# Kernel tuning notes

Measured on AMD Instinct MI355X. Metric: run time of the kernel, lower is better.

The kernel has to match this reference:

```python
import jax, jax.numpy as jnp
from jax import lax
import numpy as np

STATE_DIM = 64
CHANNELS = 128
SEQ_LEN = 4096
BATCH = 16
DT_MIN, DT_MAX = 1e-3, 1e-1


def hippo(n):
    # HiPPO-LegS construction, matching the torch staticmethod
    ar = jnp.arange(n, dtype=jnp.float32)
    P = jnp.sqrt(1.0 + 2.0 * ar)
    A = P[:, None] * P[None, :]
    A = jnp.tril(A) - jnp.diag(ar)
    B = jnp.sqrt(2.0 * ar + 1.0)
    return -A, B[:, None]


def setup_inputs() -> dict:
    key = jax.random.key(0)
    k_u, k_c = jax.random.split(key)
    A, B = hippo(STATE_DIM)
    # xavier_normal_ for C: std = sqrt(2/(fan_in+fan_out))
    std = float(np.sqrt(2.0 / (CHANNELS + STATE_DIM)))
    C = jax.random.normal(k_c, (CHANNELS, STATE_DIM), dtype=jnp.float32) * std
    D = jnp.ones((CHANNELS, 1), dtype=jnp.float32)
    # deterministic dt at log-midpoint of [dt_min, dt_max]
    dt = jnp.exp(jnp.array([(np.log(DT_MIN) + np.log(DT_MAX)) / 2.0], dtype=jnp.float32))
    u = jax.random.normal(k_u, (BATCH, SEQ_LEN), dtype=jnp.float32)
    return {"u": u, "A": A, "B": B, "C": C, "D": D, "dt": dt}


def reference(u, A, B, C, D, dt):
    # Training-path forward of LinearStateSpaceLayer (conv-kernel construction + conv1d)
    b, L = u.shape
    n = A.shape[0]
    dt_s = dt[0]
    I = jnp.eye(n, dtype=A.dtype)
    BL = jnp.linalg.inv(I - 0.5 * dt_s * A)            # bilinear discretization
    A_bar = BL @ (I + 0.5 * dt_s * A)                  # (n, n)
    B_bar = (BL * dt_s) @ B                            # (n, 1)

    # kernel k[j] = C @ A_bar^j @ B_bar for j = 0..L-1, via a scan of matvecs
    def step(v, _):
        return A_bar @ v, v
    _, vs = lax.scan(step, B_bar[:, 0], None, length=L)  # (L, n), vs[j] = A_bar^j B_bar
    k_causal = vs @ C.T                                  # (L, channels)
    # torch ordering: k_conv[c, 0, i] = C A_bar^{L-1-i} B_bar = k_causal[L-1-i, c]
    k_conv = k_causal[::-1].T[:, None, :]                # (channels, 1, L)

    # torch F.conv1d is cross-correlation; lax conv_general_dilated matches
    y = lax.conv_general_dilated(
        u[:, None, :], k_conv,
        window_strides=(1,), padding=[(L - 1, L - 1)],
        dimension_numbers=("NCH", "OIH", "NCH"),
    )[:, :, :L]                                          # (b, channels, L)

    # skip term: (u.unsqueeze(-1) @ D.T).transpose(-1,-2) == u[b,t] * D[c,0]
    y = y + u[:, None, :] * D[None, :, :]                # (b, channels, L)
    return y
```

## Files before the change

### kernel.cpp

```cpp
#include <hip/hip_runtime.h>

#define NS   64
#define CH   128
#define LSEQ 4096
#define NB   16
#define SCH  64
#define MCH  64
#define ST   68
#define CT_ST 132

#define WS_ABAR 0
#define WS_A16  4096
#define WS_VS   8192
#define WS_BBAR 12288

#define X0_IDX(b, m) (((size_t)(b) * CH) * LSEQ + (size_t)(m) * SCH)

#define FMA44(av, bv)                                                          \
    a0.x += av.x * bv.x; a0.y += av.x * bv.y; a0.z += av.x * bv.z; a0.w += av.x * bv.w; \
    a1.x += av.y * bv.x; a1.y += av.y * bv.y; a1.z += av.y * bv.z; a1.w += av.y * bv.w; \
    a2.x += av.z * bv.x; a2.y += av.z * bv.y; a2.z += av.z * bv.z; a2.w += av.z * bv.w; \
    a3.x += av.w * bv.x; a3.y += av.w * bv.y; a3.z += av.w * bv.z; a3.w += av.w * bv.w;

__global__ __launch_bounds__(256) void k_sb(const float* __restrict__ u,
                                            const float* __restrict__ A,
                                            const float* __restrict__ Bv,
                                            const float* __restrict__ dtp,
                                            float* __restrict__ ws,
                                            float* __restrict__ out) {
    __shared__ __align__(16) float Mrow[NS * ST];
    __shared__ __align__(16) float Mcol[(NS + 1) * ST];
    __shared__ __align__(16) float Nrow[NS * ST];
    __shared__ __align__(16) float Ncol[NS * ST];
    __shared__ __align__(16) float VT[NS * ST];
    __shared__ __align__(16) float vsS[NS * NS];
    __shared__ __align__(16) float xleS[MCH * NS];
    __shared__ __align__(16) float part[2][4 * NS];
    __shared__ __align__(16) float bcol[NS];
    __shared__ float rdiag[NS], xcS[NS], vtmp[NS];
    const int tid = threadIdx.x;
    const int b = blockIdx.x;
    const float dt = dtp[0];
    const float hdt = 0.5f * dt;

    for (int o = tid; o < NS * ST; o += 256) { Mrow[o] = 0.f; Nrow[o] = 0.f; Ncol[o] = 0.f; VT[o] = 0.f; }
    for (int o = tid; o < (NS + 1) * ST; o += 256) Mcol[o] = 0.f;
    __syncthreads();

    for (int o = tid; o < NS * NS; o += 256) {
        int i = o >> 6, k = o & 63;
        float a = A[o];
        float d = (i == k) ? 1.0f : 0.0f;
        Nrow[i * ST + k] = d - hdt * a;
        Ncol[k * ST + i] = d + hdt * a;
    }
    if (tid < NS) bcol[tid] = dt * Bv[tid];
    __syncthreads();
    if (tid < NS) rdiag[tid] = 1.0f / Nrow[tid * ST + tid];
    __syncthreads();

    if (tid <= NS) {
        const int j = tid;
        float* xrow = &Mcol[j * ST];
        for (int I = 0; I < 16; ++I) {
            const int i0 = 4 * I;
            float4 t2 = (j < NS) ? *(const float4*)&Ncol[j * ST + i0]
                                 : *(const float4*)&bcol[i0];
            float a0 = t2.x, a1 = t2.y, a2 = t2.z, a3 = t2.w;
            for (int k = 0; k < i0; k += 4) {
                float4 xk = *(const float4*)&xrow[k];
                float4 n0 = *(const float4*)&Nrow[(i0 + 0) * ST + k];
                float4 n1 = *(const float4*)&Nrow[(i0 + 1) * ST + k];
                float4 n2 = *(const float4*)&Nrow[(i0 + 2) * ST + k];
                float4 n3 = *(const float4*)&Nrow[(i0 + 3) * ST + k];
                a0 -= n0.x * xk.x + n0.y * xk.y + n0.z * xk.z + n0.w * xk.w;
                a1 -= n1.x * xk.x + n1.y * xk.y + n1.z * xk.z + n1.w * xk.w;
                a2 -= n2.x * xk.x + n2.y * xk.y + n2.z * xk.z + n2.w * xk.w;
                a3 -= n3.x * xk.x + n3.y * xk.y + n3.z * xk.z + n3.w * xk.w;
            }
            float4 rd  = *(const float4*)&rdiag[i0];
            float4 nb1 = *(const float4*)&Nrow[(i0 + 1) * ST + i0];
            float4 nb2 = *(const float4*)&Nrow[(i0 + 2) * ST + i0];
            float4 nb3 = *(const float4*)&Nrow[(i0 + 3) * ST + i0];
            float x0 = a0 * rd.x;
            float x1 = (a1 - nb1.x * x0) * rd.y;
            float x2 = (a2 - nb2.x * x0 - nb2.y * x1) * rd.z;
            float x3 = (a3 - nb3.x * x0 - nb3.y * x1 - nb3.z * x2) * rd.w;
            float4 xw = {x0, x1, x2, x3};
            *(float4*)&xrow[i0] = xw;
        }
    }
    __syncthreads();

    {
        const int i0 = 4 * (tid >> 4), j0 = 4 * (tid & 15);
        float4 r0 = *(const float4*)&Mcol[(j0 + 0) * ST + i0];
        float4 r1 = *(const float4*)&Mcol[(j0 + 1) * ST + i0];
        float4 r2 = *(const float4*)&Mcol[(j0 + 2) * ST + i0];
        float4 r3 = *(const float4*)&Mcol[(j0 + 3) * ST + i0];
        float4 w0 = {r0.x, r1.x, r2.x, r3.x};
        float4 w1 = {r0.y, r1.y, r2.y, r3.y};
        float4 w2 = {r0.z, r1.z, r2.z, r3.z};
        float4 w3 = {r0.w, r1.w, r2.w, r3.w};
        *(float4*)&Mrow[(i0 + 0) * ST + j0] = w0;
        *(float4*)&Mrow[(i0 + 1) * ST + j0] = w1;
        *(float4*)&Mrow[(i0 + 2) * ST + j0] = w2;
        *(float4*)&Mrow[(i0 + 3) * ST + j0] = w3;
        if (b == 0) {
            *(float4*)&ws[WS_ABAR + (i0 + 0) * NS + j0] = w0;
            *(float4*)&ws[WS_ABAR + (i0 + 1) * NS + j0] = w1;
            *(float4*)&ws[WS_ABAR + (i0 + 2) * NS + j0] = w2;
            *(float4*)&ws[WS_ABAR + (i0 + 3) * NS + j0] = w3;
        }
    }
    if (b == 0 && tid < 16)
        *(float4*)&ws[WS_BBAR + 4 * tid] = *(const float4*)&Mcol[NS * ST + 4 * tid];
    __syncthreads();

    if ((tid >> 6) == 0) {
        const int i = tid;
        float v = Mcol[NS * ST + i];
        vtmp[i] = v;
        VT[i * ST + 0] = v;
        for (int j = 1; j < 4; ++j) {
            __threadfence_block();
            float s = 0.f;
            for (int k = 0; k < NS; k += 4) {
                float4 ar = *(const float4*)&Mrow[i * ST + k];
                float4 vv = *(const float4*)&vtmp[k];
                s += ar.x * vv.x + ar.y * vv.y + ar.z * vv.z + ar.w * vv.w;
            }
            __threadfence_block();
            vtmp[i] = s;
            VT[i * ST + j] = s;
        }
    }
    __syncthreads();

    float *cm = Mrow, *cmt = Mcol, *nm = Nrow, *nmt = Ncol;
    const int w4 = tid >> 6, l = tid & 63;
    const int si0 = 16 * w4 + 4 * (l >> 4);
    const int sj0 = 4 * (l & 15);
    const int skmax = 16 * (w4 + 1);
    for (int s = 1; s <= 6; ++s) {
        {
            float4 a0 = {0,0,0,0}, a1 = {0,0,0,0}, a2 = {0,0,0,0}, a3 = {0,0,0,0};
            for (int k = 0; k < skmax; k += 4) {
                float4 av0 = *(const float4*)&cmt[(k + 0) * ST + si0];
                float4 bv0 = *(const float4*)&cm [(k + 0) * ST + sj0];
                float4 av1 = *(const float4*)&cmt[(k + 1) * ST + si0];
                float4 bv1 = *(const float4*)&cm [(k + 1) * ST + sj0];
                float4 av2 = *(const float4*)&cmt[(k + 2) * ST + si0];
                float4 bv2 = *(const float4*)&cm [(k + 2) * ST + sj0];
                float4 av3 = *(const float4*)&cmt[(k + 3) * ST + si0];
                float4 bv3 = *(const float4*)&cm [(k + 3) * ST + sj0];
                FMA44(av0, bv0)
                FMA44(av1, bv1)
                FMA44(av2, bv2)
                FMA44(av3, bv3)
            }
            *(float4*)&nm[(si0 + 0) * ST + sj0] = a0;
            *(float4*)&nm[(si0 + 1) * ST + sj0] = a1;
            *(float4*)&nm[(si0 + 2) * ST + sj0] = a2;
            *(float4*)&nm[(si0 + 3) * ST + sj0] = a3;
            float4 t0 = {a0.x, a1.x, a2.x, a3.x};
            float4 t1 = {a0.y, a1.y, a2.y, a3.y};
            float4 t2 = {a0.z, a1.z, a2.z, a3.z};
            float4 t3 = {a0.w, a1.w, a2.w, a3.w};
            *(float4*)&nmt[(sj0 + 0) * ST + si0] = t0;
            *(float4*)&nmt[(sj0 + 1) * ST + si0] = t1;
            *(float4*)&nmt[(sj0 + 2) * ST + si0] = t2;
            *(float4*)&nmt[(sj0 + 3) * ST + si0] = t3;
        }
        __syncthreads();
        { float* t = cm; cm = nm; nm = t; t = cmt; cmt = nmt; nmt = t; }
        if (s == 4 && b == 0) {
            for (int o = tid; o < (NS * NS) / 4; o += 256) {
                int r = o >> 4, c4 = (o & 15) * 4;
                *(float4*)&ws[WS_A16 + r * NS + c4] = *(const float4*)&cm[r * ST + c4];
            }
        }
        if (s >= 2 && s <= 5) {
            const int m = 1 << s;
            if (tid < 4 * m) {
                const int vi = 4 * (tid & 15), vj = 4 * (tid >> 4);
                float4 a0 = {0,0,0,0}, a1 = {0,0,0,0}, a2 = {0,0,0,0}, a3 = {0,0,0,0};
                for (int k = 0; k < NS; k += 2) {
                    float4 av  = *(const float4*)&cmt[k * ST + vi];
                    float4 bv  = *(const float4*)&VT [k * ST + vj];
                    float4 av2 = *(const float4*)&cmt[(k + 1) * ST + vi];
                    float4 bv2 = *(const float4*)&VT [(k + 1) * ST + vj];
                    FMA44(av, bv)
                    FMA44(av2, bv2)
                }
                *(float4*)&VT[(vi + 0) * ST + vj + m] = a0;
                *(float4*)&VT[(vi + 1) * ST + vj + m] = a1;
                *(float4*)&VT[(vi + 2) * ST + vj + m] = a2;
                *(float4*)&VT[(vi + 3) * ST + vj + m] = a3;
            }
        }
        __syncthreads();
    }

    {
        const int it = tid >> 4, jt = tid & 15;
        const int i0 = 4 * it, j0 = 4 * jt;
        float4 v0 = *(const float4*)&VT[(i0 + 0) * ST + j0];
        float4 v1 = *(const float4*)&VT[(i0 + 1) * ST + j0];
        float4 v2 = *(const float4*)&VT[(i0 + 2) * ST + j0];
        float4 v3 = *(const float4*)&VT[(i0 + 3) * ST + j0];
        float4 w0 = {v0.x, v1.x, v2.x, v3.x};
        float4 w1 = {v0.y, v1.y, v2.y, v3.y};
        float4 w2 = {v0.z, v1.z, v2.z, v3.z};
        float4 w3 = {v0.w, v1.w, v2.w, v3.w};
        *(float4*)&vsS[(j0 + 0) * NS + i0] = w0;
        *(float4*)&vsS[(j0 + 1) * NS + i0] = w1;
        *(float4*)&vsS[(j0 + 2) * NS + i0] = w2;
        *(float4*)&vsS[(j0 + 3) * NS + i0] = w3;
        if (b == 0) {
            *(float4*)&ws[WS_VS + (j0 + 0) * NS + i0] = w0;
            *(float4*)&ws[WS_VS + (j0 + 1) * NS + i0] = w1;
            *(float4*)&ws[WS_VS + (j0 + 2) * NS + i0] = w2;
            *(float4*)&ws[WS_VS + (j0 + 3) * NS + i0] = w3;
        }
    }

    {
        const int jj = tid & 63;
        for (int rep = 0; rep < 4; ++rep) {
            const int m0 = 4 * (tid >> 6) + 16 * rep;
            float4 v;
            v.x = u[b * LSEQ + (m0 + 0) * SCH + 63 - jj];
            v.y = u[b * LSEQ + (m0 + 1) * SCH + 63 - jj];
            v.z = u[b * LSEQ + (m0 + 2) * SCH + 63 - jj];
            v.w = u[b * LSEQ + (m0 + 3) * SCH + 63 - jj];
            *(float4*)&Nrow[jj * ST + m0] = v;
        }
    }
    const int i = tid & 63, q = tid >> 6;
    float4 a64[4];
#pragma unroll
    for (int kq = 0; kq < 4; ++kq)
        a64[kq] = *(const float4*)&Mrow[i * ST + 16 * q + 4 * kq];
    __syncthreads();

    {
        const int ig = tid & 15, mg = tid >> 4;
        float4 a0 = {0,0,0,0}, a1 = {0,0,0,0}, a2 = {0,0,0,0}, a3 = {0,0,0,0};
        for (int j = 0; j < NS; j += 2) {
            float4 am  = *(const float4*)&Nrow[j * ST + 4 * mg];
            float4 bi  = *(const float4*)&vsS[j * NS + 4 * ig];
            float4 am2 = *(const float4*)&Nrow[(j + 1) * ST + 4 * mg];
            float4 bi2 = *(const float4*)&vsS[(j + 1) * NS + 4 * ig];
            FMA44(am, bi)
            FMA44(am2, bi2)
        }
        *(float4*)&xleS[(4 * mg + 0) * NS + 4 * ig] = a0;
        *(float4*)&xleS[(4 * mg + 1) * NS + 4 * ig] = a1;
        *(float4*)&xleS[(4 * mg + 2) * NS + 4 * ig] = a2;
        *(float4*)&xleS[(4 * mg + 3) * NS + 4 * ig] = a3;
    }
    if (tid < NS) xcS[tid] = 0.f;
    __syncthreads();

    for (int m = 0; m < MCH; ++m) {
        if (q == 0) out[X0_IDX(b, m) + i] = xcS[i];
        float4 t0 = *(const float4*)(xcS + 16 * q + 0);
        float4 t1 = *(const float4*)(xcS + 16 * q + 4);
        float4 t2 = *(const float4*)(xcS + 16 * q + 8);
        float4 t3 = *(const float4*)(xcS + 16 * q + 12);
        float s = a64[0].x * t0.x + a64[0].y * t0.y + a64[0].z * t0.z + a64[0].w * t0.w
                + a64[1].x * t1.x + a64[1].y * t1.y + a64[1].z * t1.z + a64[1].w * t1.w
                + a64[2].x * t2.x + a64[2].y * t2.y + a64[2].z * t2.z + a64[2].w * t2.w
                + a64[3].x * t3.x + a64[3].y * t3.y + a64[3].z * t3.z + a64[3].w * t3.w;
        part[m & 1][q * 64 + i] = s;
        __syncthreads();
        float xn = part[m & 1][i] + part[m & 1][64 + i] + part[m & 1][128 + i]
                 + part[m & 1][192 + i] + xleS[m * 64 + i];
        xcS[i] = xn;
    }
}

__global__ __launch_bounds__(256) void k_main2(const float* __restrict__ u,
                                               const float* __restrict__ Cm,
                                               const float* __restrict__ Dv,
                                               const float* __restrict__ ws,
                                               float* __restrict__ out) {
    __shared__ __align__(16) float Xl[NS * ST];
    __shared__ __align__(16) float CtS[NS * CT_ST];
    __shared__ __align__(16) float xcW[4 * NS];
    __shared__ __align__(16) float xbS[4 * NS];
    __shared__ __align__(16) float VSS[16 * NS];
    __shared__ __align__(16) float pleS[4 * NS];
    __shared__ __align__(16) float partS[4 * NS];
    __shared__ float uS[SCH], DS[CH], bbS[NS];
    const int m = blockIdx.x, b = blockIdx.y;
    const int tid = threadIdx.x;
    const int l = tid & 63, w = tid >> 6;

    for (int o = tid; o < (NS * NS) / 4; o += 256) {
        int r = o >> 4, c4 = (o & 15) * 4;
        *(float4*)&Xl[r * ST + c4]     = *(const float4*)&ws[WS_ABAR + r * NS + c4];
        *(float4*)&CtS[r * CT_ST + c4] = *(const float4*)&ws[WS_A16 + r * NS + c4];
    }
    for (int o = tid; o < 16 * NS; o += 256) VSS[o] = ws[WS_VS + o];
    if (tid < NS) {
        uS[tid]  = u[b * LSEQ + m * SCH + tid];
        bbS[tid] = ws[WS_BBAR + tid];
        xbS[tid] = out[X0_IDX(b, m) + tid];
    }
    if (tid < CH) DS[tid] = Dv[tid];
    __syncthreads();

    const int r0 = l & 15, q = l >> 4;
    float4 ar[4][4];
#pragma unroll
    for (int b4 = 0; b4 < 4; ++b4)
#pragma unroll
        for (int kq = 0; kq < 4; ++kq)
            ar[b4][kq] = *(const float4*)&Xl[(r0 + 16 * b4) * ST + 16 * q + 4 * kq];
    float bbr[4];
#pragma unroll
    for (int b4 = 0; b4 < 4; ++b4) bbr[b4] = bbS[r0 + 16 * b4];
    float4 a16r[4];
#pragma unroll
    for (int kq = 0; kq < 4; ++kq)
        a16r[kq] = *(const float4*)&CtS[l * CT_ST + 16 * w + 4 * kq];

    {
        float s = 0.f;
#pragma unroll
        for (int j = 0; j < 16; ++j) s += VSS[j * NS + l] * uS[16 * w + 15 - j];
        pleS[w * NS + l] = s;
    }
    __syncthreads();

    for (int p = 1; p < 4; ++p) {
        float4 x0q = *(const float4*)&xbS[(p - 1) * NS + 16 * w + 0];
        float4 x1q = *(const float4*)&xbS[(p - 1) * NS + 16 * w + 4];
        float4 x2q = *(const float4*)&xbS[(p - 1) * NS + 16 * w + 8];
        float4 x3q = *(const float4*)&xbS[(p - 1) * NS + 16 * w + 12];
        float s = a16r[0].x * x0q.x + a16r[0].y * x0q.y + a16r[0].z * x0q.z + a16r[0].w * x0q.w
                + a16r[1].x * x1q.x + a16r[1].y * x1q.y + a16r[1].z * x1q.z + a16r[1].w * x1q.w
                + a16r[2].x * x2q.x + a16r[2].y * x2q.y + a16r[2].z * x2q.z + a16r[2].w * x2q.w
                + a16r[3].x * x3q.x + a16r[3].y * x3q.y + a16r[3].z * x3q.z + a16r[3].w * x3q.w;
        partS[w * NS + l] = s;
        __syncthreads();
        if (w == 0) {
            float xn = partS[l] + partS[NS + l] + partS[2 * NS + l] + partS[3 * NS + l]
                     + pleS[(p - 1) * NS + l];
            xbS[p * NS + l] = xn;
        }
        __syncthreads();
    }

    xcW[w * NS + l] = xbS[w * NS + l];
    for (int s = 0; s < 16; ++s) {
        __threadfence_block();
        const int t = 16 * w + s;
        float4 x0q = *(const float4*)&xcW[w * NS + 16 * q + 0];
        float4 x1q = *(const float4*)&xcW[w * NS + 16 * q + 4];
        float4 x2q = *(const float4*)&xcW[w * NS + 16 * q + 8];
        float4 x3q = *(const float4*)&xcW[w * NS + 16 * q + 12];
        float p0, p1, p2, p3;
        p0 = ar[0][0].x * x0q.x + ar[0][0].y * x0q.y + ar[0][0].z * x0q.z + ar[0][0].w * x0q.w
           + ar[0][1].x * x1q.x + ar[0][1].y * x1q.y + ar[0][1].z * x1q.z + ar[0][1].w * x1q.w
           + ar[0][2].x * x2q.x + ar[0][2].y * x2q.y + ar[0][2].z * x2q.z + ar[0][2].w * x2q.w
           + ar[0][3].x * x3q.x + ar[0][3].y * x3q.y + ar[0][3].z * x3q.z + ar[0][3].w * x3q.w;
        p1 = ar[1][0].x * x0q.x + ar[1][0].y * x0q.y + ar[1][0].z * x0q.z + ar[1][0].w * x0q.w
           + ar[1][1].x * x1q.x + ar[1][1].y * x1q.y + ar[1][1].z * x1q.z + ar[1][1].w * x1q.w
           + ar[1][2].x * x2q.x + ar[1][2].y * x2q.y + ar[1][2].z * x2q.z + ar[1][2].w * x2q.w
           + ar[1][3].x * x3q.x + ar[1][3].y * x3q.y + ar[1][3].z * x3q.z + ar[1][3].w * x3q.w;
        p2 = ar[2][0].x * x0q.x + ar[2][0].y * x0q.y + ar[2][0].z * x0q.z + ar[2][0].w * x0q.w
           + ar[2][1].x * x1q.x + ar[2][1].y * x1q.y + ar[2][1].z * x1q.z + ar[2][1].w * x1q.w
           + ar[2][2].x * x2q.x + ar[2][2].y * x2q.y + ar[2][2].z * x2q.z + ar[2][2].w * x2q.w
           + ar[2][3].x * x3q.x + ar[2][3].y * x3q.y + ar[2][3].z * x3q.z + ar[2][3].w * x3q.w;
        p3 = ar[3][0].x * x0q.x + ar[3][0].y * x0q.y + ar[3][0].z * x0q.z + ar[3][0].w * x0q.w
           + ar[3][1].x * x1q.x + ar[3][1].y * x1q.y + ar[3][1].z * x1q.z + ar[3][1].w * x1q.w
           + ar[3][2].x * x2q.x + ar[3][2].y * x2q.y + ar[3][2].z * x2q.z + ar[3][2].w * x2q.w
           + ar[3][3].x * x3q.x + ar[3][3].y * x3q.y + ar[3][3].z * x3q.z + ar[3][3].w * x3q.w;
        p0 += __shfl_xor(p0, 16, 64); p1 += __shfl_xor(p1, 16, 64);
        p2 += __shfl_xor(p2, 16, 64); p3 += __shfl_xor(p3, 16, 64);
        p0 += __shfl_xor(p0, 32, 64); p1 += __shfl_xor(p1, 32, 64);
        p2 += __shfl_xor(p2, 32, 64); p3 += __shfl_xor(p3, 32, 64);
        const float ut = uS[t];
        p0 += bbr[0] * ut; p1 += bbr[1] * ut; p2 += bbr[2] * ut; p3 += bbr[3] * ut;
        const float xv = (q == 0) ? p0 : (q == 1) ? p1 : (q == 2) ? p2 : p3;
        const int row = r0 + 16 * q;
        xcW[w * NS + row] = xv;
        Xl[row * ST + t]  = xv;
    }
    __syncthreads();

    for (int rep = 0; rep < 8; ++rep) {
        const int ii = tid & 63;
        const int cg = (tid >> 6) + 4 * rep;
        float4 v;
        v.x = Cm[(4 * cg + 0) * NS + ii];
        v.y = Cm[(4 * cg + 1) * NS + ii];
        v.z = Cm[(4 * cg + 2) * NS + ii];
        v.w = Cm[(4 * cg + 3) * NS + ii];
        *(float4*)&CtS[ii * CT_ST + 4 * cg] = v;
    }
    __syncthreads();

    {
        const int tg = tid & 7, cq = tid >> 3;
        float acc[4][8];
#pragma unroll
        for (int r = 0; r < 4; ++r)
#pragma unroll
            for (int c = 0; c < 8; ++c) acc[r][c] = 0.f;
#pragma unroll 4
        for (int ii = 0; ii < NS; ++ii) {
            float4 cv = *(const float4*)&CtS[ii * CT_ST + 4 * cq];
            float4 xa = *(const float4*)&Xl[ii * ST + 8 * tg + 0];
            float4 xb = *(const float4*)&Xl[ii * ST + 8 * tg + 4];
            float cr[4] = {cv.x, cv.y, cv.z, cv.w};
            float xv[8] = {xa.x, xa.y, xa.z, xa.w, xb.x, xb.y, xb.z, xb.w};
#pragma unroll
            for (int r = 0; r < 4; ++r)
#pragma unroll
                for (int c = 0; c < 8; ++c) acc[r][c] += cr[r] * xv[c];
        }
        const size_t obase = ((size_t)b * CH) * LSEQ + (size_t)m * SCH + 8 * tg;
#pragma unroll
        for (int r = 0; r < 4; ++r) {
            const int c = 4 * cq + r;
            const float dv = DS[c];
            float4 o1, o2;
            o1.x = acc[r][0] + dv * uS[8 * tg + 0];
            o1.y = acc[r][1] + dv * uS[8 * tg + 1];
            o1.z = acc[r][2] + dv * uS[8 * tg + 2];
            o1.w = acc[r][3] + dv * uS[8 * tg + 3];
            o2.x = acc[r][4] + dv * uS[8 * tg + 4];
            o2.y = acc[r][5] + dv * uS[8 * tg + 5];
            o2.z = acc[r][6] + dv * uS[8 * tg + 6];
            o2.w = acc[r][7] + dv * uS[8 * tg + 7];
            float* op = out + obase + (size_t)c * LSEQ;
            *(float4*)(op)     = o1;
            *(float4*)(op + 4) = o2;
        }
    }
}

extern "C" void kernel_launch(void* const* d_in, const int* in_sizes, int n_in,
                              void* d_out, int out_size, void* d_ws, size_t ws_size,
                              hipStream_t stream) {
    const float* u   = (const float*)d_in[0];
    const float* A   = (const float*)d_in[1];
    const float* Bv  = (const float*)d_in[2];
    const float* Cm  = (const float*)d_in[3];
    const float* Dv  = (const float*)d_in[4];
    const float* dtp = (const float*)d_in[5];
    float* ws  = (float*)d_ws;
    float* out = (float*)d_out;

    k_sb<<<NB, 256, 0, stream>>>(u, A, Bv, dtp, ws, out);
    k_main2<<<dim3(MCH, NB), 256, 0, stream>>>(u, Cm, Dv, ws, out);
}
```

Measured before the change: 167.7 us.

## Overlap Krylov vector build with matrix squaring using extra warps in setup kernel

The setup kernel goes to 512 threads. The upper 256 threads compute the A_bar^j B_bar columns (VT) while the lower 256 square the matrix, which removes the serial 4-step matvec phase and one barrier per squaring step. The triangular solve now keeps its row in registers, and the diagonal reciprocal is computed straight from A. In the second kernel several shared buffers are aliased into one pool to cut LDS use, at the cost of losing the padded stride for the C-transpose tile, which may add bank conflicts.

```diff
diff --git a/kernel.cpp b/kernel.cpp
--- a/kernel.cpp
+++ b/kernel.cpp
@@ -7,7 +7,7 @@
 #define SCH  64
 #define MCH  64
 #define ST   68
-#define CT_ST 132
+#define CP   128
 
 #define WS_ABAR 0
 #define WS_A16  4096
@@ -15,6 +15,13 @@
 #define WS_BBAR 12288
 
 #define X0_IDX(b, m) (((size_t)(b) * CH) * LSEQ + (size_t)(m) * SCH)
+
+#define P_VSS  0
+#define P_XCW  1024
+#define P_XBS  1280
+#define P_PLE  1536
+#define P_PART 1792
+#define P_A16  2048
 
 #define FMA44(av, bv)                                                          \
     a0.x += av.x * bv.x; a0.y += av.x * bv.y; a0.z += av.x * bv.z; a0.w += av.x * bv.w; \
@@ -22,7 +29,7 @@
     a2.x += av.z * bv.x; a2.y += av.z * bv.y; a2.z += av.z * bv.z; a2.w += av.z * bv.w; \
     a3.x += av.w * bv.x; a3.y += av.w * bv.y; a3.z += av.w * bv.z; a3.w += av.w * bv.w;
 
-__global__ __launch_bounds__(256) void k_sb(const float* __restrict__ u,
+__global__ __launch_bounds__(512) void k_sb(const float* __restrict__ u,
                                             const float* __restrict__ A,
                                             const float* __restrict__ Bv,
                                             const float* __restrict__ dtp,
@@ -37,46 +44,47 @@
     __shared__ __align__(16) float xleS[MCH * NS];
     __shared__ __align__(16) float part[2][4 * NS];
     __shared__ __align__(16) float bcol[NS];
-    __shared__ float rdiag[NS], xcS[NS], vtmp[NS];
+    __shared__ float rdiag[NS], xcS[NS];
     const int tid = threadIdx.x;
     const int b = blockIdx.x;
     const float dt = dtp[0];
     const float hdt = 0.5f * dt;
 
-    for (int o = tid; o < NS * ST; o += 256) { Mrow[o] = 0.f; Nrow[o] = 0.f; Ncol[o] = 0.f; VT[o] = 0.f; }
-    for (int o = tid; o < (NS + 1) * ST; o += 256) Mcol[o] = 0.f;
-    __syncthreads();
-
-    for (int o = tid; o < NS * NS; o += 256) {
+    for (int o = tid; o < NS * ST; o += 512) { Mrow[o] = 0.f; Nrow[o] = 0.f; Ncol[o] = 0.f; VT[o] = 0.f; }
+    for (int o = tid; o < (NS + 1) * ST; o += 512) Mcol[o] = 0.f;
+    __syncthreads();
+
+    for (int o = tid; o < NS * NS; o += 512) {
         int i = o >> 6, k = o & 63;
         float a = A[o];
         float d = (i == k) ? 1.0f : 0.0f;
         Nrow[i * ST + k] = d - hdt * a;
         Ncol[k * ST + i] = d + hdt * a;
     }
-    if (tid < NS) bcol[tid] = dt * Bv[tid];
-    __syncthreads();
-    if (tid < NS) rdiag[tid] = 1.0f / Nrow[tid * ST + tid];
+    if (tid < NS) {
+        bcol[tid]  = dt * Bv[tid];
+        rdiag[tid] = 1.0f / (1.0f - hdt * A[tid * NS + tid]);
+    }
     __syncthreads();
 
     if (tid <= NS) {
-        const int j = tid;
-        float* xrow = &Mcol[j * ST];
+        float xr[NS];
+        const float* t2b = (tid < NS) ? &Ncol[tid * ST] : bcol;
+#pragma unroll
         for (int I = 0; I < 16; ++I) {
             const int i0 = 4 * I;
-            float4 t2 = (j < NS) ? *(const float4*)&Ncol[j * ST + i0]
-                                 : *(const float4*)&bcol[i0];
+            float4 t2 = *(const float4*)&t2b[i0];
             float a0 = t2.x, a1 = t2.y, a2 = t2.z, a3 = t2.w;
+#pragma unroll
             for (int k = 0; k < i0; k += 4) {
-                float4 xk = *(const float4*)&xrow[k];
                 float4 n0 = *(const float4*)&Nrow[(i0 + 0) * ST + k];
                 float4 n1 = *(const float4*)&Nrow[(i0 + 1) * ST + k];
                 float4 n2 = *(const float4*)&Nrow[(i0 + 2) * ST + k];
                 float4 n3 = *(const float4*)&Nrow[(i0 + 3) * ST + k];
-                a0 -= n0.x * xk.x + n0.y * xk.y + n0.z * xk.z + n0.w * xk.w;
-                a1 -= n1.x * xk.x + n1.y * xk.y + n1.z * xk.z + n1.w * xk.w;
-                a2 -= n2.x * xk.x + n2.y * xk.y + n2.z * xk.z + n2.w * xk.w;
-                a3 -= n3.x * xk.x + n3.y * xk.y + n3.z * xk.z + n3.w * xk.w;
+                a0 -= n0.x * xr[k] + n0.y * xr[k + 1] + n0.z * xr[k + 2] + n0.w * xr[k + 3];
+                a1 -= n1.x * xr[k] + n1.y * xr[k + 1] + n1.z * xr[k + 2] + n1.w * xr[k + 3];
+                a2 -= n2.x * xr[k] + n2.y * xr[k + 1] + n2.z * xr[k + 2] + n2.w * xr[k + 3];
+                a3 -= n3.x * xr[k] + n3.y * xr[k + 1] + n3.z * xr[k + 2] + n3.w * xr[k + 3];
             }
             float4 rd  = *(const float4*)&rdiag[i0];
             float4 nb1 = *(const float4*)&Nrow[(i0 + 1) * ST + i0];
@@ -86,13 +94,18 @@
             float x1 = (a1 - nb1.x * x0) * rd.y;
             float x2 = (a2 - nb2.x * x0 - nb2.y * x1) * rd.z;
             float x3 = (a3 - nb3.x * x0 - nb3.y * x1 - nb3.z * x2) * rd.w;
-            float4 xw = {x0, x1, x2, x3};
-            *(float4*)&xrow[i0] = xw;
-        }
-    }
-    __syncthreads();
-
-    {
+            xr[i0 + 0] = x0; xr[i0 + 1] = x1; xr[i0 + 2] = x2; xr[i0 + 3] = x3;
+        }
+        float* xrow = &Mcol[tid * ST];
+#pragma unroll
+        for (int k = 0; k < NS; k += 4) {
+            float4 v = {xr[k], xr[k + 1], xr[k + 2], xr[k + 3]};
+            *(float4*)&xrow[k] = v;
+        }
+    }
+    __syncthreads();
+
+    if (tid < 256) {
         const int i0 = 4 * (tid >> 4), j0 = 4 * (tid & 15);
         float4 r0 = *(const float4*)&Mcol[(j0 + 0) * ST + i0];
         float4 r1 = *(const float4*)&Mcol[(j0 + 1) * ST + i0];
@@ -115,37 +128,18 @@
     }
     if (b == 0 && tid < 16)
         *(float4*)&ws[WS_BBAR + 4 * tid] = *(const float4*)&Mcol[NS * ST + 4 * tid];
-    __syncthreads();
-
-    if ((tid >> 6) == 0) {
-        const int i = tid;
-        float v = Mcol[NS * ST + i];
-        vtmp[i] = v;
-        VT[i * ST + 0] = v;
-        for (int j = 1; j < 4; ++j) {
-            __threadfence_block();
-            float s = 0.f;
+    if (tid < NS) VT[tid * ST + 0] = Mcol[NS * ST + tid];
+    __syncthreads();
+
+    float *cm = Mrow, *cmt = Mcol, *nm = Nrow, *nmt = Ncol;
+    const int l = tid & 63;
+    const int si0 = 16 * ((tid >> 6) & 3) + 4 * (l >> 4);
+    const int sj0 = 4 * (l & 15);
+    for (int s = 1; s <= 6; ++s) {
+        if (tid < 256) {
+            float4 a0 = {0,0,0,0}, a1 = {0,0,0,0}, a2 = {0,0,0,0}, a3 = {0,0,0,0};
+#pragma unroll 4
             for (int k = 0; k < NS; k += 4) {
-                float4 ar = *(const float4*)&Mrow[i * ST + k];
-                float4 vv = *(const float4*)&vtmp[k];
-                s += ar.x * vv.x + ar.y * vv.y + ar.z * vv.z + ar.w * vv.w;
-            }
-            __threadfence_block();
-            vtmp[i] = s;
-            VT[i * ST + j] = s;
-        }
-    }
-    __syncthreads();
-
-    float *cm = Mrow, *cmt = Mcol, *nm = Nrow, *nmt = Ncol;
-    const int w4 = tid >> 6, l = tid & 63;
-    const int si0 = 16 * w4 + 4 * (l >> 4);
-    const int sj0 = 4 * (l & 15);
-    const int skmax = 16 * (w4 + 1);
-    for (int s = 1; s <= 6; ++s) {
-        {
-            float4 a0 = {0,0,0,0}, a1 = {0,0,0,0}, a2 = {0,0,0,0}, a3 = {0,0,0,0};
-            for (int k = 0; k < skmax; k += 4) {
                 float4 av0 = *(const float4*)&cmt[(k + 0) * ST + si0];
                 float4 bv0 = *(const float4*)&cm [(k + 0) * ST + sj0];
                 float4 av1 = *(const float4*)&cmt[(k + 1) * ST + si0];
@@ -171,40 +165,56 @@
             *(float4*)&nmt[(sj0 + 1) * ST + si0] = t1;
             *(float4*)&nmt[(sj0 + 2) * ST + si0] = t2;
             *(float4*)&nmt[(sj0 + 3) * ST + si0] = t3;
+        } else {
+            const int e = tid - 256;
+            if (s == 1) {
+                if (e < NS) {
+                    float sum = 0.f;
+#pragma unroll 8
+                    for (int k = 0; k < NS; ++k) sum += cmt[k * ST + e] * VT[k * ST + 0];
+                    VT[e * ST + 1] = sum;
+                }
+            } else if (s == 2) {
+                if (e < 2 * NS) {
+                    const int i = e & 63, j = e >> 6;
+                    float sum = 0.f;
+#pragma unroll 8
+                    for (int k = 0; k < NS; ++k) sum += cmt[k * ST + i] * VT[k * ST + j];
+                    VT[i * ST + 2 + j] = sum;
+                }
+            } else {
+                const int mexp = 1 << (s - 1);
+                if (e < 4 * mexp) {
+                    const int vi = 4 * (e & 15), vj = 4 * (e >> 4);
+                    float4 a0 = {0,0,0,0}, a1 = {0,0,0,0}, a2 = {0,0,0,0}, a3 = {0,0,0,0};
+#pragma unroll 4
+                    for (int k = 0; k < NS; k += 2) {
+                        float4 av  = *(const float4*)&cmt[k * ST + vi];
+                        float4 bv  = *(const float4*)&VT [k * ST + vj];
+                        float4 av2 = *(const float4*)&cmt[(k + 1) * ST + vi];
+                        float4 bv2 = *(const float4*)&VT [(k + 1) * ST + vj];
+                        FMA44(av, bv)
+                        FMA44(av2, bv2)
+                    }
+                    *(float4*)&VT[(vi + 0) * ST + vj + mexp] = a0;
+                    *(float4*)&VT[(vi + 1) * ST + vj + mexp] = a1;
+                    *(float4*)&VT[(vi + 2) * ST + vj + mexp] = a2;
+                    *(float4*)&VT[(vi + 3) * ST + vj + mexp] = a3;
+                }
+            }
         }
         __syncthreads();
         { float* t = cm; cm = nm; nm = t; t = cmt; cmt = nmt; nmt = t; }
         if (s == 4 && b == 0) {
-            for (int o = tid; o < (NS * NS) / 4; o += 256) {
+            for (int o = tid; o < (NS * NS) / 4; o += 512) {
                 int r = o >> 4, c4 = (o & 15) * 4;
                 *(float4*)&ws[WS_A16 + r * NS + c4] = *(const float4*)&cm[r * ST + c4];
             }
         }
-        if (s >= 2 && s <= 5) {
-            const int m = 1 << s;
-            if (tid < 4 * m) {
-                const int vi = 4 * (tid & 15), vj = 4 * (tid >> 4);
-                float4 a0 = {0,0,0,0}, a1 = {0,0,0,0}, a2 = {0,0,0,0}, a3 = {0,0,0,0};
-                for (int k = 0; k < NS; k += 2) {
-                    float4 av  = *(const float4*)&cmt[k * ST + vi];
-                    float4 bv  = *(const float4*)&VT [k * ST + vj];
-                    float4 av2 = *(const float4*)&cmt[(k + 1) * ST + vi];
-                    float4 bv2 = *(const float4*)&VT [(k + 1) * ST + vj];
-                    FMA44(av, bv)
-                    FMA44(av2, bv2)
-                }
-                *(float4*)&VT[(vi + 0) * ST + vj + m] = a0;
-                *(float4*)&VT[(vi + 1) * ST + vj + m] = a1;
-                *(float4*)&VT[(vi + 2) * ST + vj + m] = a2;
-                *(float4*)&VT[(vi + 3) * ST + vj + m] = a3;
-            }
-        }
-        __syncthreads();
-    }
-
-    {
-        const int it = tid >> 4, jt = tid & 15;
-        const int i0 = 4 * it, j0 = 4 * jt;
+    }
+
+    if (tid < 256) {
+        const int i0 = 4 * (tid >> 4), j0 = 4 * (tid & 15);
         float4 v0 = *(const float4*)&VT[(i0 + 0) * ST + j0];
         float4 v1 = *(const float4*)&VT[(i0 + 1) * ST + j0];
         float4 v2 = *(const float4*)&VT[(i0 + 2) * ST + j0];
@@ -224,11 +234,11 @@
             *(float4*)&ws[WS_VS + (j0 + 3) * NS + i0] = w3;
         }
     }
-
     {
         const int jj = tid & 63;
-        for (int rep = 0; rep < 4; ++rep) {
-            const int m0 = 4 * (tid >> 6) + 16 * rep;
+#pragma unroll
+        for (int rep = 0; rep < 2; ++rep) {
+            const int m0 = 4 * (tid >> 6) + 32 * rep;
             float4 v;
             v.x = u[b * LSEQ + (m0 + 0) * SCH + 63 - jj];
             v.y = u[b * LSEQ + (m0 + 1) * SCH + 63 - jj];
@@ -237,16 +247,20 @@
             *(float4*)&Nrow[jj * ST + m0] = v;
         }
     }
-    const int i = tid & 63, q = tid >> 6;
+    const int i = tid & 63, q = (tid >> 6) & 3;
     float4 a64[4];
-#pragma unroll
-    for (int kq = 0; kq < 4; ++kq)
-        a64[kq] = *(const float4*)&Mrow[i * ST + 16 * q + 4 * kq];
-    __syncthreads();
-
-    {
+    if (tid < 256) {
+#pragma unroll
+        for (int kq = 0; kq < 4; ++kq)
+            a64[kq] = *(const float4*)&Mrow[i * ST + 16 * q + 4 * kq];
+    }
+    if (tid < NS) xcS[tid] = 0.f;
+    __syncthreads();
+
+    if (tid < 256) {
         const int ig = tid & 15, mg = tid >> 4;
         float4 a0 = {0,0,0,0}, a1 = {0,0,0,0}, a2 = {0,0,0,0}, a3 = {0,0,0,0};
+#pragma unroll 4
         for (int j = 0; j < NS; j += 2) {
             float4 am  = *(const float4*)&Nrow[j * ST + 4 * mg];
             float4 bi  = *(const float4*)&vsS[j * NS + 4 * ig];
@@ -260,24 +274,27 @@
         *(float4*)&xleS[(4 * mg + 2) * NS + 4 * ig] = a2;
         *(float4*)&xleS[(4 * mg + 3) * NS + 4 * ig] = a3;
     }
-    if (tid < NS) xcS[tid] = 0.f;
     __syncthreads();
 
     for (int m = 0; m < MCH; ++m) {
-        if (q == 0) out[X0_IDX(b, m) + i] = xcS[i];
-        float4 t0 = *(const float4*)(xcS + 16 * q + 0);
-        float4 t1 = *(const float4*)(xcS + 16 * q + 4);
-        float4 t2 = *(const float4*)(xcS + 16 * q + 8);
-        float4 t3 = *(const float4*)(xcS + 16 * q + 12);
-        float s = a64[0].x * t0.x + a64[0].y * t0.y + a64[0].z * t0.z + a64[0].w * t0.w
-                + a64[1].x * t1.x + a64[1].y * t1.y + a64[1].z * t1.z + a64[1].w * t1.w
-                + a64[2].x * t2.x + a64[2].y * t2.y + a64[2].z * t2.z + a64[2].w * t2.w
-                + a64[3].x * t3.x + a64[3].y * t3.y + a64[3].z * t3.z + a64[3].w * t3.w;
-        part[m & 1][q * 64 + i] = s;
+        if (tid < 256) {
+            if (q == 0 && tid < 64) out[X0_IDX(b, m) + i] = xcS[i];
+            float4 t0 = *(const float4*)(xcS + 16 * q + 0);
+            float4 t1 = *(const float4*)(xcS + 16 * q + 4);
+            float4 t2 = *(const float4*)(xcS + 16 * q + 8);
+            float4 t3 = *(const float4*)(xcS + 16 * q + 12);
+            float s = a64[0].x * t0.x + a64[0].y * t0.y + a64[0].z * t0.z + a64[0].w * t0.w
+                    + a64[1].x * t1.x + a64[1].y * t1.y + a64[1].z * t1.z + a64[1].w * t1.w
+                    + a64[2].x * t2.x + a64[2].y * t2.y + a64[2].z * t2.z + a64[2].w * t2.w
+                    + a64[3].x * t3.x + a64[3].y * t3.y + a64[3].z * t3.z + a64[3].w * t3.w;
+            part[m & 1][q * 64 + i] = s;
+        }
         __syncthreads();
-        float xn = part[m & 1][i] + part[m & 1][64 + i] + part[m & 1][128 + i]
-                 + part[m & 1][192 + i] + xleS[m * 64 + i];
-        xcS[i] = xn;
+        if (tid < 256) {
+            float xn = part[m & 1][i] + part[m & 1][64 + i] + part[m & 1][128 + i]
+                     + part[m & 1][192 + i] + xleS[m * 64 + i];
+            xcS[i] = xn;
+        }
     }
 }
 
@@ -287,12 +304,7 @@
                                                const float* __restrict__ ws,
                                                float* __restrict__ out) {
     __shared__ __align__(16) float Xl[NS * ST];
-    __shared__ __align__(16) float CtS[NS * CT_ST];
-    __shared__ __align__(16) float xcW[4 * NS];
-    __shared__ __align__(16) float xbS[4 * NS];
-    __shared__ __align__(16) float VSS[16 * NS];
-    __shared__ __align__(16) float pleS[4 * NS];
-    __shared__ __align__(16) float partS[4 * NS];
+    __shared__ __align__(16) float pool[NS * CP];
     __shared__ float uS[SCH], DS[CH], bbS[NS];
     const int m = blockIdx.x, b = blockIdx.y;
     const int tid = threadIdx.x;
@@ -300,14 +312,14 @@
 
     for (int o = tid; o < (NS * NS) / 4; o += 256) {
         int r = o >> 4, c4 = (o & 15) * 4;
-        *(float4*)&Xl[r * ST + c4]     = *(const float4*)&ws[WS_ABAR + r * NS + c4];
-        *(float4*)&CtS[r * CT_ST + c4] = *(const float4*)&ws[WS_A16 + r * NS + c4];
-    }
-    for (int o = tid; o < 16 * NS; o += 256) VSS[o] = ws[WS_VS + o];
+        *(float4*)&Xl[r * ST + c4]          = *(const float4*)&ws[WS_ABAR + r * NS + c4];
+        *(float4*)&pool[P_A16 + r * NS + c4] = *(const float4*)&ws[WS_A16 + r * NS + c4];
+    }
+    for (int o = tid; o < 16 * NS; o += 256) pool[P_VSS + o] = ws[WS_VS + o];
     if (tid < NS) {
         uS[tid]  = u[b * LSEQ + m * SCH + tid];
         bbS[tid] = ws[WS_BBAR + tid];
-        xbS[tid] = out[X0_IDX(b, m) + tid];
+        pool[P_XBS + tid] = out[X0_IDX(b, m) + tid];
     }
     if (tid < CH) DS[tid] = Dv[tid];
     __syncthreads();
@@ -325,43 +337,43 @@
     float4 a16r[4];
 #pragma unroll
     for (int kq = 0; kq < 4; ++kq)
-        a16r[kq] = *(const float4*)&CtS[l * CT_ST + 16 * w + 4 * kq];
+        a16r[kq] = *(const float4*)&pool[P_A16 + l * NS + 16 * w + 4 * kq];
 
     {
         float s = 0.f;
 #pragma unroll
-        for (int j = 0; j < 16; ++j) s += VSS[j * NS + l] * uS[16 * w + 15 - j];
-        pleS[w * NS + l] = s;
+        for (int j = 0; j < 16; ++j) s += pool[P_VSS + j * NS + l] * uS[16 * w + 15 - j];
+        pool[P_PLE + w * NS + l] = s;
     }
     __syncthreads();
 
     for (int p = 1; p < 4; ++p) {
-        float4 x0q = *(const float4*)&xbS[(p - 1) * NS + 16 * w + 0];
-        float4 x1q = *(const float4*)&xbS[(p - 1) * NS + 16 * w + 4];
-        float4 x2q = *(const float4*)&xbS[(p - 1) * NS + 16 * w + 8];
-        float4 x3q = *(const float4*)&xbS[(p - 1) * NS + 16 * w + 12];
+        float4 x0q = *(const float4*)&pool[P_XBS + (p - 1) * NS + 16 * w + 0];
+        float4 x1q = *(const float4*)&pool[P_XBS + (p - 1) * NS + 16 * w + 4];
+        float4 x2q = *(const float4*)&pool[P_XBS + (p - 1) * NS + 16 * w + 8];
+        float4 x3q = *(const float4*)&pool[P_XBS + (p - 1) * NS + 16 * w + 12];
         float s = a16r[0].x * x0q.x + a16r[0].y * x0q.y + a16r[0].z * x0q.z + a16r[0].w * x0q.w
                 + a16r[1].x * x1q.x + a16r[1].y * x1q.y + a16r[1].z * x1q.z + a16r[1].w * x1q.w
                 + a16r[2].x * x2q.x + a16r[2].y * x2q.y + a16r[2].z * x2q.z + a16r[2].w * x2q.w
                 + a16r[3].x * x3q.x + a16r[3].y * x3q.y + a16r[3].z * x3q.z + a16r[3].w * x3q.w;
-        partS[w * NS + l] = s;
+        pool[P_PART + w * NS + l] = s;
         __syncthreads();
         if (w == 0) {
-            float xn = partS[l] + partS[NS + l] + partS[2 * NS + l] + partS[3 * NS + l]
-                     + pleS[(p - 1) * NS + l];
-            xbS[p * NS + l] = xn;
+            float xn = pool[P_PART + l] + pool[P_PART + NS + l] + pool[P_PART + 2 * NS + l]
+                     + pool[P_PART + 3 * NS + l] + pool[P_PLE + (p - 1) * NS + l];
+            pool[P_XBS + p * NS + l] = xn;
         }
         __syncthreads();
     }
 
-    xcW[w * NS + l] = xbS[w * NS + l];
+    pool[P_XCW + w * NS + l] = pool[P_XBS + w * NS + l];
     for (int s = 0; s < 16; ++s) {
         __threadfence_block();
         const int t = 16 * w + s;
-        float4 x0q = *(const float4*)&xcW[w * NS + 16 * q + 0];
-        float4 x1q = *(const float4*)&xcW[w * NS + 16 * q + 4];
-        float4 x2q = *(const float4*)&xcW[w * NS + 16 * q + 8];
-        float4 x3q = *(const float4*)&xcW[w * NS + 16 * q + 12];
+        float4 x0q = *(const float4*)&pool[P_XCW + w * NS + 16 * q + 0];
+        float4 x1q = *(const float4*)&pool[P_XCW + w * NS + 16 * q + 4];
+        float4 x2q = *(const float4*)&pool[P_XCW + w * NS + 16 * q + 8];
+        float4 x3q = *(const float4*)&pool[P_XCW + w * NS + 16 * q + 12];
         float p0, p1, p2, p3;
         p0 = ar[0][0].x * x0q.x + ar[0][0].y * x0q.y + ar[0][0].z * x0q.z + ar[0][0].w * x0q.w
            + ar[0][1].x * x1q.x + ar[0][1].y * x1q.y + ar[0][1].z * x1q.z + ar[0][1].w * x1q.w
@@ -387,11 +399,12 @@
         p0 += bbr[0] * ut; p1 += bbr[1] * ut; p2 += bbr[2] * ut; p3 += bbr[3] * ut;
         const float xv = (q == 0) ? p0 : (q == 1) ? p1 : (q == 2) ? p2 : p3;
         const int row = r0 + 16 * q;
-        xcW[w * NS + row] = xv;
-        Xl[row * ST + t]  = xv;
-    }
-    __syncthreads();
-
+        pool[P_XCW + w * NS + row] = xv;
+        Xl[row * ST + t] = xv;
+    }
+    __syncthreads();
+
+#pragma unroll
     for (int rep = 0; rep < 8; ++rep) {
         const int ii = tid & 63;
         const int cg = (tid >> 6) + 4 * rep;
@@ -400,7 +413,7 @@
         v.y = Cm[(4 * cg + 1) * NS + ii];
         v.z = Cm[(4 * cg + 2) * NS + ii];
         v.w = Cm[(4 * cg + 3) * NS + ii];
-        *(float4*)&CtS[ii * CT_ST + 4 * cg] = v;
+        *(float4*)&pool[ii * CP + 4 * cg] = v;
     }
     __syncthreads();
 
@@ -413,7 +426,7 @@
             for (int c = 0; c < 8; ++c) acc[r][c] = 0.f;
 #pragma unroll 4
         for (int ii = 0; ii < NS; ++ii) {
-            float4 cv = *(const float4*)&CtS[ii * CT_ST + 4 * cq];
+            float4 cv = *(const float4*)&pool[ii * CP + 4 * cq];
             float4 xa = *(const float4*)&Xl[ii * ST + 8 * tg + 0];
             float4 xb = *(const float4*)&Xl[ii * ST + 8 * tg + 4];
             float cr[4] = {cv.x, cv.y, cv.z, cv.w};
@@ -456,6 +469,6 @@
     float* ws  = (float*)d_ws;
     float* out = (float*)d_out;
 
-    k_sb<<<NB, 256, 0, stream>>>(u, A, Bv, dtp, ws, out);
+    k_sb<<<NB, 512, 0, stream>>>(u, A, Bv, dtp, ws, out);
     k_main2<<<dim3(MCH, NB), 256, 0, stream>>>(u, Cm, Dv, ws, out);
 }
```

Result: faster. 160.4 us (-4.3%).
